# Kernel tuning notes

Measured on AMD Instinct MI355X. Metric: run time of the kernel, lower is better.

## Reference

```python
import jax, jax.numpy as jnp
import numpy as np

KV_POOL = 2


def setup_inputs() -> dict:
    key = jax.random.key(0)
    ks = jax.random.split(key, 12)
    B, C1, C2, H, W, D = 8, 256, 512, 64, 64, 64
    s = 0.02
    return {
        "x1": jax.random.normal(ks[0], (B, C1, H, W), jnp.float32),
        "x2": jax.random.normal(ks[1], (B, C2, H, W), jnp.float32),
        "Wq": jax.random.normal(ks[2], (D, C1), jnp.float32) * s,
        "bq": jnp.zeros((D,), jnp.float32),
        "Wk": jax.random.normal(ks[3], (D, C2), jnp.float32) * s,
        "bk": jnp.zeros((D,), jnp.float32),
        "Wv": jax.random.normal(ks[4], (D, C2), jnp.float32) * s,
        "bv": jnp.zeros((D,), jnp.float32),
        "Wo": jax.random.normal(ks[5], (C1, D), jnp.float32) * s,
        "bo": jnp.zeros((C1,), jnp.float32),
    }


def reference(x1, x2, Wq, bq, Wk, bk, Wv, bv, Wo, bo):
    B, C1, H, W = x1.shape
    D = Wq.shape[0]
    # adaptive_avg_pool2d to (H//2, W//2) with even dims == 2x2 mean pool
    Bs, C2, H2, W2 = x2.shape
    x2p = x2.reshape(Bs, C2, H2 // KV_POOL, KV_POOL, W2 // KV_POOL, KV_POOL).mean(axis=(3, 5))
    # 1x1 convs as channel matmuls; flatten spatial dims
    Q = jnp.einsum('bchw,dc->bhwd', x1, Wq).reshape(B, H * W, D) + bq          # [B,N,D]
    K = jnp.einsum('bchw,dc->bhwd', x2p, Wk).reshape(B, -1, D) + bk            # [B,M,D]
    V = jnp.einsum('bchw,dc->bhwd', x2p, Wv).reshape(B, -1, D) + bv            # [B,M,D]
    attn = jax.nn.softmax(jnp.einsum('bnd,bmd->bnm', Q, K), axis=-1)           # [B,N,M]
    out = jnp.einsum('bnm,bmd->bnd', attn, V)                                  # [B,N,D]
    y = jnp.einsum('bnd,cd->bnc', out, Wo) + bo                                # [B,N,C1]
    y = y.reshape(B, H, W, C1).transpose(0, 3, 1, 2)                           # [B,C1,H,W]
    return x1 + y
```

## Files before the change

### kernel.cpp

```cpp
#include <hip/hip_runtime.h>
#include <hip/hip_bf16.h>

typedef __bf16 bf16x2 __attribute__((ext_vector_type(2)));
typedef __bf16 bf16x4 __attribute__((ext_vector_type(4)));
typedef __bf16 bf16x8 __attribute__((ext_vector_type(8)));
typedef float f32x16 __attribute__((ext_vector_type(16)));
typedef unsigned int u32x4 __attribute__((ext_vector_type(4)));

static constexpr int Bc = 8, C1 = 256, C2 = 512, Hh = 64, Ww = 64, Dd = 64;
static constexpr int Nn = 4096, Mm = 1024;

#define MFMA __builtin_amdgcn_mfma_f32_32x32x16_bf16

__device__ __forceinline__ uint32_t pkbf(float a, float b) {
  union { __bf16 h[2]; uint32_t u; } x;
  x.h[0] = (__bf16)a; x.h[1] = (__bf16)b;
  return x.u;
}

__device__ __forceinline__ bf16x8 cvt8(const float* __restrict__ p) {
  float4 a = *(const float4*)p;
  float4 b2 = *(const float4*)(p + 4);
  bf16x8 r;
  r[0] = (__bf16)a.x; r[1] = (__bf16)a.y; r[2] = (__bf16)a.z; r[3] = (__bf16)a.w;
  r[4] = (__bf16)b2.x; r[5] = (__bf16)b2.y; r[6] = (__bf16)b2.z; r[7] = (__bf16)b2.w;
  return r;
}

__device__ __forceinline__ void pack16(const float* p, bf16x8& f0, bf16x8& f1) {
  uint32_t w01 = pkbf(p[0], p[1]),   w23 = pkbf(p[2], p[3]);
  uint32_t w45 = pkbf(p[4], p[5]),   w67 = pkbf(p[6], p[7]);
  uint32_t w89 = pkbf(p[8], p[9]),   wab = pkbf(p[10], p[11]);
  uint32_t wcd = pkbf(p[12], p[13]), wef = pkbf(p[14], p[15]);
  auto s0 = __builtin_amdgcn_permlane32_swap(w01, w45, false, false);
  auto s1 = __builtin_amdgcn_permlane32_swap(w23, w67, false, false);
  auto s2 = __builtin_amdgcn_permlane32_swap(w89, wcd, false, false);
  auto s3 = __builtin_amdgcn_permlane32_swap(wab, wef, false, false);
  u32x4 q0 = {s0[0], s1[0], s0[1], s1[1]};
  u32x4 q1 = {s2[0], s3[0], s2[1], s3[1]};
  f0 = __builtin_bit_cast(bf16x8, q0);
  f1 = __builtin_bit_cast(bf16x8, q1);
}


__global__ __launch_bounds__(256) void k_stage(
    const float* __restrict__ x1, const float* __restrict__ x2,
    const float* __restrict__ Wq, const float* __restrict__ Wk,
    const float* __restrict__ Wv, const float* __restrict__ Wo,
    __bf16* __restrict__ wqf, __bf16* __restrict__ wkf,
    __bf16* __restrict__ wvf, __bf16* __restrict__ wof,
    __bf16* __restrict__ x1f, __bf16* __restrict__ x2pf) {
  __shared__ __align__(16) __bf16 lds[16 * 516];
  const int lin = blockIdx.x, tid = threadIdx.x;
  const int w = tid >> 6, l = tid & 63;

  if (lin >= 1536) {
    int t = (lin - 1536) * 256 + tid;
    if (t < 2048) {
      int ll = t & 63, g = t >> 6, dh = g >> 4, ks = g & 15;
      int d = dh * 32 + (ll & 31), c = ks * 16 + (ll >> 5) * 8;
      *(bf16x8*)(wqf + (size_t)t * 8) = cvt8(Wq + (size_t)d * C1 + c);
    } else if (t < 6144) {
      int tt = t - 2048;
      int ll = tt & 63, g = tt >> 6, dh = g >> 5, ks = g & 31;
      int d = dh * 32 + (ll & 31), c = ks * 16 + (ll >> 5) * 8;
      *(bf16x8*)(wkf + (size_t)tt * 8) = cvt8(Wk + (size_t)d * C2 + c);
    } else if (t < 10240) {
      int tt = t - 6144;
      int ll = tt & 63, g = tt >> 6, dh = g >> 5, ks = g & 31;
      int d = dh * 32 + (ll & 31), c = ks * 16 + (ll >> 5) * 8;
      *(bf16x8*)(wvf + (size_t)tt * 8) = cvt8(Wv + (size_t)d * C2 + c);
    } else if (t < 12288) {
      int tt = t - 10240;
      int ll = tt & 63, g = tt >> 6, ct = g >> 2, ks = g & 3;
      int crow = ct * 32 + (ll & 31), d = ks * 16 + (ll >> 5) * 8;
      *(bf16x8*)(wof + (size_t)tt * 8) = cvt8(Wo + (size_t)crow * Dd + d);
    }
    return;
  }

  if (lin < 512) {
    const int b = lin & 7, q = lin >> 3;
    const int ks2 = q & 31, half = q >> 5;
#pragma unroll
    for (int cc = 0; cc < 4; ++cc) {
      const int c_loc = w * 4 + cc;
      const int c = ks2 * 16 + c_loc;
      const float* src = x2 + ((size_t)(b * C2 + c) * Hh + half * 32) * Ww;
      float4 v[8];
#pragma unroll
      for (int it = 0; it < 8; ++it)
        v[it] = *(const float4*)(src + it * 256 + l * 4);
#pragma unroll
      for (int it = 0; it < 8; ++it) {
        float s0 = v[it].x + v[it].y, s1 = v[it].z + v[it].w;
        float p0 = (s0 + __shfl_xor(s0, 16)) * 0.25f;
        float p1 = (s1 + __shfl_xor(s1, 16)) * 0.25f;
        const int rl = l >> 4;
        if ((rl & 1) == 0) {
          int h2l = it * 2 + (rl >> 1);
          bf16x2 pv; pv[0] = (__bf16)p0; pv[1] = (__bf16)p1;
          *(bf16x2*)(lds + c_loc * 516 + h2l * 32 + 2 * (l & 15)) = pv;
        }
      }
    }
    __syncthreads();
#pragma unroll
    for (int ti = 0; ti < 4; ++ti) {
      const int t_loc = w * 4 + ti;
      bf16x8 f;
#pragma unroll
      for (int e = 0; e < 8; ++e)
        f[e] = lds[((l >> 5) * 8 + e) * 516 + t_loc * 32 + (l & 31)];
      const int t_m = half * 16 + t_loc;
      *(bf16x8*)(x2pf + ((size_t)(b * 32 + t_m) * 32 + ks2) * 512 + l * 8) = f;
    }
  } else {
    const int e0 = lin - 512;
    const int b = e0 & 7, r = e0 >> 3;
    const int ks = r & 15, nch = r >> 4;
    const int n0 = nch * 512;
    float4 v[8];
#pragma unroll
    for (int cc = 0; cc < 4; ++cc) {
      const float* src = x1 + (size_t)(b * C1 + ks * 16 + w * 4 + cc) * Nn + n0;
#pragma unroll
      for (int j = 0; j < 2; ++j)
        v[cc * 2 + j] = *(const float4*)(src + j * 256 + l * 4);
    }
#pragma unroll
    for (int cc = 0; cc < 4; ++cc) {
      const int c_loc = w * 4 + cc;
#pragma unroll
      for (int j = 0; j < 2; ++j) {
        float4 vv = v[cc * 2 + j];
        bf16x4 t4;
        t4[0] = (__bf16)vv.x; t4[1] = (__bf16)vv.y;
        t4[2] = (__bf16)vv.z; t4[3] = (__bf16)vv.w;
        *(bf16x4*)(lds + c_loc * 516 + j * 256 + l * 4) = t4;
      }
    }
    __syncthreads();
#pragma unroll
    for (int ti = 0; ti < 4; ++ti) {
      const int t_loc = w * 4 + ti;
      bf16x8 f;
#pragma unroll
      for (int e = 0; e < 8; ++e)
        f[e] = lds[((l >> 5) * 8 + e) * 516 + t_loc * 32 + (l & 31)];
      const int t = nch * 16 + t_loc;
      *(bf16x8*)(x1f + ((size_t)(b * 128 + t) * 16 + ks) * 512 + l * 8) = f;
    }
  }
}

__global__ __launch_bounds__(256) void k_proj(
    const __bf16* __restrict__ x1f, const __bf16* __restrict__ x2pf,
    const __bf16* __restrict__ wqf, const float* __restrict__ bq,
    const __bf16* __restrict__ wkf, const float* __restrict__ bk,
    const __bf16* __restrict__ wvf, const float* __restrict__ bv,
    __bf16* __restrict__ qfb, __bf16* __restrict__ kfb,
    __bf16* __restrict__ vfb) {
  const int lin = blockIdx.x;
  const int b = lin & 7, idx = lin >> 3;
  const int tid = threadIdx.x;
  const int w = tid >> 6, l = tid & 63, h = l >> 5, nl = l & 31;

  if (idx < 64) {
    const int nsub = w & 1, dh = w >> 1;
    const int t = idx * 2 + nsub;
    const __bf16* af = x1f + ((size_t)(b * 128 + t) * 16) * 512 + l * 8;
    const __bf16* wf = wqf + (size_t)dh * 16 * 512 + l * 8;
    f32x16 acc = {};
#pragma unroll
    for (int ks = 0; ks < 16; ++ks) {
      bf16x8 a = *(const bf16x8*)(af + ks * 512);
      bf16x8 bb = *(const bf16x8*)(wf + ks * 512);
      acc = MFMA(a, bb, acc, 0, 0, 0);
    }
    const int d = dh * 32 + nl;
    const float bias = bq[d];
    __bf16* qdst = qfb + (size_t)b * Nn * Dd + (size_t)t * 2048 +
                   (d >> 4) * 512 + ((d >> 3) & 1) * 256 + (d & 7);
#pragma unroll
    for (int r = 0; r < 16; ++r) {
      int mrow = (r & 3) + 8 * (r >> 2) + 4 * h;
      qdst[mrow * 8] = (__bf16)(acc[r] + bias);
    }
  } else {
    const int h2 = idx - 64;
    const int isv = w >> 1, dh = w & 1;
    const __bf16* af = x2pf + ((size_t)(b * 32 + h2) * 32) * 512 + l * 8;
    const __bf16* wf = (isv ? wvf : wkf) + (size_t)dh * 32 * 512 + l * 8;
    f32x16 acc = {};
#pragma unroll
    for (int ks = 0; ks < 32; ++ks) {
      bf16x8 a = *(const bf16x8*)(af + ks * 512);
      bf16x8 bb = *(const bf16x8*)(wf + ks * 512);
      acc = MFMA(a, bb, acc, 0, 0, 0);
    }
    const int d = dh * 32 + nl;
    if (!isv) {
      const float bias = bk[d];
      __bf16* kdst = kfb + (size_t)b * Mm * Dd + (size_t)h2 * 2048 +
                     (d >> 4) * 512 + ((d >> 3) & 1) * 256 + (d & 7);
#pragma unroll
      for (int r = 0; r < 16; ++r) {
        int mr = (r & 3) + 8 * (r >> 2) + 4 * h;
        kdst[mr * 8] = (__bf16)(acc[r] + bias);
      }
    } else {
      const float bias = bv[d];
      float ov[16];
#pragma unroll
      for (int r = 0; r < 16; ++r) ov[r] = acc[r] + bias;
      bf16x8 f0, f1;
      pack16(ov, f0, f1);
      __bf16* vdst = vfb + (size_t)b * Mm * Dd + (size_t)h2 * 2048 + l * 8;
      *(bf16x8*)(vdst + (size_t)dh * 512) = f0;
      *(bf16x8*)(vdst + (size_t)(2 + dh) * 512) = f1;
    }
  }
}

template <int S>
__global__ __launch_bounds__(256) void k_attn_part(
    const __bf16* __restrict__ qfb, const __bf16* __restrict__ kfb,
    const __bf16* __restrict__ vfb, __bf16* __restrict__ po,
    float* __restrict__ pml) {
  const int lin = blockIdx.x;
  const int b = lin & 7, rest = lin >> 3, nblk = rest & 31, sp = rest >> 5;
  const int tid = threadIdx.x;
  const int w = tid >> 6, l = tid & 63, h = l >> 5, nl = l & 31;
  const int n = nblk * 128 + w * 32 + nl;
  constexpr int NT = Mm / S / 32;
  const int t0 = sp * NT;

  const __bf16* qt = qfb + (size_t)b * Nn * Dd + (size_t)(nblk * 4 + w) * 2048 + l * 8;
  bf16x8 qf0 = *(const bf16x8*)(qt);
  bf16x8 qf1 = *(const bf16x8*)(qt + 512);
  bf16x8 qf2 = *(const bf16x8*)(qt + 1024);
  bf16x8 qf3 = *(const bf16x8*)(qt + 1536);

  const __bf16* kt = kfb + (size_t)b * Mm * Dd + (size_t)t0 * 2048 + l * 8;
  const __bf16* vt = vfb + (size_t)b * Mm * Dd + (size_t)t0 * 2048 + l * 8;

  f32x16 o0 = {}, o1 = {};
  float lsum = 0.f;

  bf16x8 ck0 = *(const bf16x8*)(kt);
  bf16x8 ck1 = *(const bf16x8*)(kt + 512);
  bf16x8 ck2 = *(const bf16x8*)(kt + 1024);
  bf16x8 ck3 = *(const bf16x8*)(kt + 1536);
  bf16x8 cv0 = *(const bf16x8*)(vt);
  bf16x8 cv1 = *(const bf16x8*)(vt + 512);
  bf16x8 cv2 = *(const bf16x8*)(vt + 1024);
  bf16x8 cv3 = *(const bf16x8*)(vt + 1536);

#pragma unroll
  for (int i = 0; i < NT; ++i) {
    bf16x8 nk0, nk1, nk2, nk3, nv0, nv1, nv2, nv3;
    if (i + 1 < NT) {
      const __bf16* kn = kt + (size_t)(i + 1) * 2048;
      const __bf16* vn = vt + (size_t)(i + 1) * 2048;
      nk0 = *(const bf16x8*)(kn);
      nk1 = *(const bf16x8*)(kn + 512);
      nk2 = *(const bf16x8*)(kn + 1024);
      nk3 = *(const bf16x8*)(kn + 1536);
      nv0 = *(const bf16x8*)(vn);
      nv1 = *(const bf16x8*)(vn + 512);
      nv2 = *(const bf16x8*)(vn + 1024);
      nv3 = *(const bf16x8*)(vn + 1536);
    }
    f32x16 s = {};
    s = MFMA(ck0, qf0, s, 0, 0, 0);
    s = MFMA(ck1, qf1, s, 0, 0, 0);
    s = MFMA(ck2, qf2, s, 0, 0, 0);
    s = MFMA(ck3, qf3, s, 0, 0, 0);
    float p[16];
#pragma unroll
    for (int r = 0; r < 16; ++r) p[r] = __expf(s[r]);
    float u0 = (p[0] + p[1]) + (p[2] + p[3]);
    float u1 = (p[4] + p[5]) + (p[6] + p[7]);
    float u2 = (p[8] + p[9]) + (p[10] + p[11]);
    float u3 = (p[12] + p[13]) + (p[14] + p[15]);
    lsum += (u0 + u1) + (u2 + u3);
    bf16x8 pb0, pb1;
    pack16(p, pb0, pb1);
    o0 = MFMA(cv0, pb0, o0, 0, 0, 0);
    o1 = MFMA(cv1, pb0, o1, 0, 0, 0);
    o0 = MFMA(cv2, pb1, o0, 0, 0, 0);
    o1 = MFMA(cv3, pb1, o1, 0, 0, 0);
    if (i + 1 < NT) {
      ck0 = nk0; ck1 = nk1; ck2 = nk2; ck3 = nk3;
      cv0 = nv0; cv1 = nv1; cv2 = nv2; cv3 = nv3;
    }
  }

  const float ltot = lsum + __shfl_xor(lsum, 32);
  __bf16* ob = po + (size_t)(b * S + sp) * 16 * Nn * 4 + (size_t)n * 4;
#pragma unroll
  for (int q = 0; q < 4; ++q) {
    bf16x4 t0v, t1v;
#pragma unroll
    for (int e = 0; e < 4; ++e) {
      t0v[e] = (__bf16)o0[q * 4 + e];
      t1v[e] = (__bf16)o1[q * 4 + e];
    }
    *(bf16x4*)(ob + (size_t)(2 * q + h) * Nn * 4) = t0v;
    *(bf16x4*)(ob + (size_t)(8 + 2 * q + h) * Nn * 4) = t1v;
  }
  if (h == 0) pml[(size_t)(b * S + sp) * Nn + n] = ltot;
}

template <int S>
__global__ __launch_bounds__(256) void k_attn_comb(
    const float* __restrict__ x1, const __bf16* __restrict__ po,
    const float* __restrict__ pml, const __bf16* __restrict__ wof,
    const float* __restrict__ bo, float* __restrict__ out) {
  const int lin = blockIdx.x;
  const int b = lin & 7, rest = lin >> 3, nblk = rest & 31, ctg = rest >> 5;
  const int tid = threadIdx.x;
  const int w = tid >> 6, l = tid & 63, h = l >> 5, nl = l & 31;
  const int n = nblk * 128 + w * 32 + nl;

  float L = 0.f;
#pragma unroll
  for (int s = 0; s < S; ++s)
    L += pml[(size_t)(b * S + s) * Nn + n];
  const float inv = 1.f / L;

  float o[32];
#pragma unroll
  for (int r = 0; r < 32; ++r) o[r] = 0.f;
#pragma unroll
  for (int s = 0; s < S; ++s) {
    const __bf16* ob = po + (size_t)(b * S + s) * 16 * Nn * 4 + (size_t)n * 4;
#pragma unroll
    for (int q = 0; q < 4; ++q) {
      bf16x4 v0 = *(const bf16x4*)(ob + (size_t)(2 * q + h) * Nn * 4);
      bf16x4 v1 = *(const bf16x4*)(ob + (size_t)(8 + 2 * q + h) * Nn * 4);
#pragma unroll
      for (int e = 0; e < 4; ++e) {
        o[q * 4 + e] += (float)v0[e];
        o[16 + q * 4 + e] += (float)v1[e];
      }
    }
  }

  bf16x8 obf[4];
#pragma unroll
  for (int a2 = 0; a2 < 2; ++a2) {
    float ov[16];
#pragma unroll
    for (int r = 0; r < 16; ++r) ov[r] = o[a2 * 16 + r] * inv;
    pack16(ov, obf[a2 * 2], obf[a2 * 2 + 1]);
  }

  const float* x1r = x1 + (size_t)b * C1 * Nn + n;
  float* outr = out + (size_t)b * C1 * Nn + n;
#pragma unroll
  for (int ci = 0; ci < 4; ++ci) {
    const int ct = ctg * 4 + ci;
    f32x16 y = {};
#pragma unroll
    for (int ks = 0; ks < 4; ++ks) {
      bf16x8 a = *(const bf16x8*)(wof + (size_t)((ct * 4 + ks) * 64 + l) * 8);
      y = MFMA(a, obf[ks], y, 0, 0, 0);
    }
#pragma unroll
    for (int r = 0; r < 16; ++r) {
      int c = ct * 32 + (r & 3) + 8 * (r >> 2) + 4 * h;
      size_t idx = (size_t)c * Nn;
      outr[idx] = y[r] + bo[c] + x1r[idx];
    }
  }
}

__global__ __launch_bounds__(256) void k_attn(
    const float* __restrict__ x1, const __bf16* __restrict__ qfb,
    const __bf16* __restrict__ kfb, const __bf16* __restrict__ vfb,
    const __bf16* __restrict__ wof, const float* __restrict__ bo,
    float* __restrict__ out) {
  const int b = blockIdx.y, tid = threadIdx.x;
  const int w = tid >> 6, l = tid & 63, h = l >> 5, nl = l & 31;
  const int n = blockIdx.x * 128 + w * 32 + nl;

  const __bf16* qt = qfb + (size_t)b * Nn * Dd + (size_t)(blockIdx.x * 4 + w) * 2048 + l * 8;
  bf16x8 qf0 = *(const bf16x8*)(qt);
  bf16x8 qf1 = *(const bf16x8*)(qt + 512);
  bf16x8 qf2 = *(const bf16x8*)(qt + 1024);
  bf16x8 qf3 = *(const bf16x8*)(qt + 1536);

  f32x16 o0 = {}, o1 = {};
  float mrun = -INFINITY, lsum = 0.f;

  const __bf16* kb_ = kfb + (size_t)b * Mm * Dd + l * 8;
  const __bf16* vb_ = vfb + (size_t)b * Mm * Dd + l * 8;

  for (int t = 0; t < 32; ++t) {
    const __bf16* kt = kb_ + (size_t)t * 2048;
    const __bf16* vt = vb_ + (size_t)t * 2048;
    bf16x8 ka0 = *(const bf16x8*)(kt);
    bf16x8 ka1 = *(const bf16x8*)(kt + 512);
    bf16x8 ka2 = *(const bf16x8*)(kt + 1024);
    bf16x8 ka3 = *(const bf16x8*)(kt + 1536);
    bf16x8 v00 = *(const bf16x8*)(vt);
    bf16x8 v10 = *(const bf16x8*)(vt + 512);
    bf16x8 v01 = *(const bf16x8*)(vt + 1024);
    bf16x8 v11 = *(const bf16x8*)(vt + 1536);
    f32x16 s = {};
    s = MFMA(ka0, qf0, s, 0, 0, 0);
    s = MFMA(ka1, qf1, s, 0, 0, 0);
    s = MFMA(ka2, qf2, s, 0, 0, 0);
    s = MFMA(ka3, qf3, s, 0, 0, 0);
    float tmax = s[0];
#pragma unroll
    for (int r = 1; r < 16; ++r) tmax = fmaxf(tmax, s[r]);
    tmax = fmaxf(tmax, __shfl_xor(tmax, 32));
    const float mnew = fmaxf(mrun, tmax);
    const float scale = __expf(mrun - mnew);
    float p[16], psum = 0.f;
#pragma unroll
    for (int r = 0; r < 16; ++r) { p[r] = __expf(s[r] - mnew); psum += p[r]; }
    lsum = lsum * scale + psum;
    mrun = mnew;
#pragma unroll
    for (int r = 0; r < 16; ++r) { o0[r] *= scale; o1[r] *= scale; }
    bf16x8 pb0, pb1;
    pack16(p, pb0, pb1);
    o0 = MFMA(v00, pb0, o0, 0, 0, 0);
    o1 = MFMA(v10, pb0, o1, 0, 0, 0);
    o0 = MFMA(v01, pb1, o0, 0, 0, 0);
    o1 = MFMA(v11, pb1, o1, 0, 0, 0);
  }

  const float ltot = lsum + __shfl_xor(lsum, 32);
  const float inv = 1.f / ltot;

  bf16x8 ob[4];
#pragma unroll
  for (int a2 = 0; a2 < 2; ++a2) {
    float ov[16];
#pragma unroll
    for (int r = 0; r < 16; ++r) ov[r] = (a2 ? o1[r] : o0[r]) * inv;
    pack16(ov, ob[a2 * 2], ob[a2 * 2 + 1]);
  }

  const float* x1r = x1 + (size_t)b * C1 * Nn + n;
  float* outr = out + (size_t)b * C1 * Nn + n;
#pragma unroll 2
  for (int ct = 0; ct < 8; ++ct) {
    f32x16 y = {};
#pragma unroll
    for (int ks = 0; ks < 4; ++ks) {
      bf16x8 a = *(const bf16x8*)(wof + (size_t)((ct * 4 + ks) * 64 + l) * 8);
      y = MFMA(a, ob[ks], y, 0, 0, 0);
    }
#pragma unroll
    for (int r = 0; r < 16; ++r) {
      int c = ct * 32 + (r & 3) + 8 * (r >> 2) + 4 * h;
      size_t idx = (size_t)c * Nn;
      outr[idx] = y[r] + bo[c] + x1r[idx];
    }
  }
}

extern "C" void kernel_launch(void* const* d_in, const int* in_sizes, int n_in,
                              void* d_out, int out_size, void* d_ws,
                              size_t ws_size, hipStream_t stream) {
  const float* x1 = (const float*)d_in[0];
  const float* x2 = (const float*)d_in[1];
  const float* Wq = (const float*)d_in[2];
  const float* bq = (const float*)d_in[3];
  const float* Wk = (const float*)d_in[4];
  const float* bk = (const float*)d_in[5];
  const float* Wv = (const float*)d_in[6];
  const float* bv = (const float*)d_in[7];
  const float* Wo = (const float*)d_in[8];
  const float* bo = (const float*)d_in[9];
  float* out = (float*)d_out;
  char* ws = (char*)d_ws;

  __bf16* wqf  = (__bf16*)(ws);
  __bf16* wkf  = (__bf16*)(ws + 32768);
  __bf16* wvf  = (__bf16*)(ws + 98304);
  __bf16* wof  = (__bf16*)(ws + 163840);
  __bf16* qfb  = (__bf16*)(ws + 196608);
  __bf16* kfb  = (__bf16*)(ws + 4390912);
  __bf16* vfb  = (__bf16*)(ws + 5439488);
  __bf16* x1f  = (__bf16*)(ws + 6488064);
  __bf16* x2pf = (__bf16*)(ws + 23265280);
  __bf16* po   = (__bf16*)(ws + 31653888);
  const size_t ws8 = 31653888ull + 33554432ull + 1048576ull;
  const size_t ws4 = 31653888ull + 16777216ull + 524288ull;

  hipLaunchKernelGGL(k_stage, dim3(1584), dim3(256), 0, stream,
                     x1, x2, Wq, Wk, Wv, Wo, wqf, wkf, wvf, wof, x1f, x2pf);
  hipLaunchKernelGGL(k_proj, dim3(768), dim3(256), 0, stream,
                     x1f, x2pf, wqf, bq, wkf, bk, wvf, bv, qfb, kfb, vfb);
  if (ws_size >= ws8) {
    float* pml = (float*)(ws + 31653888 + 33554432);
    hipLaunchKernelGGL(k_attn_part<8>, dim3(32 * 8 * 8), dim3(256), 0, stream,
                       qfb, kfb, vfb, po, pml);
    hipLaunchKernelGGL(k_attn_comb<8>, dim3(32 * 8 * 2), dim3(256), 0, stream,
                       x1, po, pml, wof, bo, out);
  } else if (ws_size >= ws4) {
    float* pml = (float*)(ws + 31653888 + 16777216);
    hipLaunchKernelGGL(k_attn_part<4>, dim3(32 * 8 * 4), dim3(256), 0, stream,
                       qfb, kfb, vfb, po, pml);
    hipLaunchKernelGGL(k_attn_comb<4>, dim3(32 * 8 * 2), dim3(256), 0, stream,
                       x1, po, pml, wof, bo, out);
  } else {
    hipLaunchKernelGGL(k_attn, dim3(32, 8), dim3(256), 0, stream,
                       x1, qfb, kfb, vfb, wof, bo, out);
  }
}
```

Baseline: 66.49 us.

## Move activation transpose into projection kernel and read bf16 x1 for residual

The staging kernel now converts x1 to bf16 in its original NCHW layout and 2x2-pools x2 to bf16 NCHW with simple coalesced elementwise code, with no LDS transpose. The projection kernel loads channel-major tiles and transposes them through LDS before its MFMA loops. The attention epilogue now reads the residual x1 from this bf16 copy instead of the fp32 input, which halves the residual read traffic. In exchange the residual is rounded to bf16, which lowers output accuracy, and the scalar LDS transpose writes in the projection may cause bank conflicts.

```diff
diff --git a/kernel.cpp b/kernel.cpp
--- a/kernel.cpp
+++ b/kernel.cpp
@@ -42,20 +42,50 @@
   f1 = __builtin_bit_cast(bf16x8, q1);
 }
 
-
-__global__ __launch_bounds__(256) void k_stage(
+__global__ __launch_bounds__(256) void k_convert(
     const float* __restrict__ x1, const float* __restrict__ x2,
     const float* __restrict__ Wq, const float* __restrict__ Wk,
     const float* __restrict__ Wv, const float* __restrict__ Wo,
     __bf16* __restrict__ wqf, __bf16* __restrict__ wkf,
     __bf16* __restrict__ wvf, __bf16* __restrict__ wof,
-    __bf16* __restrict__ x1f, __bf16* __restrict__ x2pf) {
-  __shared__ __align__(16) __bf16 lds[16 * 516];
+    __bf16* __restrict__ x1bf, __bf16* __restrict__ x2p) {
   const int lin = blockIdx.x, tid = threadIdx.x;
-  const int w = tid >> 6, l = tid & 63;
-
-  if (lin >= 1536) {
-    int t = (lin - 1536) * 256 + tid;
+
+  if (lin < 1024) {
+    const int gi = lin * 256 + tid;
+    float4 v[8];
+#pragma unroll
+    for (int it = 0; it < 8; ++it)
+      v[it] = *(const float4*)(x1 + ((size_t)it * 262144 + gi) * 4);
+#pragma unroll
+    for (int it = 0; it < 8; ++it) {
+      bf16x4 t4;
+      t4[0] = (__bf16)v[it].x; t4[1] = (__bf16)v[it].y;
+      t4[2] = (__bf16)v[it].z; t4[3] = (__bf16)v[it].w;
+      *(bf16x4*)(x1bf + ((size_t)it * 262144 + gi) * 4) = t4;
+    }
+  } else if (lin < 2048) {
+    const int gi = (lin - 1024) * 256 + tid;
+    float4 v0[8], v1[8];
+#pragma unroll
+    for (int it = 0; it < 8; ++it) {
+      int pi = it * 262144 + gi;
+      int bc = pi >> 9, r = pi & 511, h2 = r >> 4, q = r & 15;
+      const float* base = x2 + (size_t)bc * 4096 + h2 * 128 + q * 4;
+      v0[it] = *(const float4*)(base);
+      v1[it] = *(const float4*)(base + 64);
+    }
+#pragma unroll
+    for (int it = 0; it < 8; ++it) {
+      int pi = it * 262144 + gi;
+      int bc = pi >> 9, r = pi & 511, h2 = r >> 4, q = r & 15;
+      float p0 = (v0[it].x + v0[it].y + v1[it].x + v1[it].y) * 0.25f;
+      float p1 = (v0[it].z + v0[it].w + v1[it].z + v1[it].w) * 0.25f;
+      bf16x2 pv; pv[0] = (__bf16)p0; pv[1] = (__bf16)p1;
+      *(bf16x2*)(x2p + (size_t)bc * 1024 + h2 * 32 + q * 2) = pv;
+    }
+  } else {
+    int t = (lin - 2048) * 256 + tid;
     if (t < 2048) {
       int ll = t & 63, g = t >> 6, dh = g >> 4, ks = g & 15;
       int d = dh * 32 + (ll & 31), c = ks * 16 + (ll >> 5) * 8;
@@ -76,110 +106,53 @@
       int crow = ct * 32 + (ll & 31), d = ks * 16 + (ll >> 5) * 8;
       *(bf16x8*)(wof + (size_t)tt * 8) = cvt8(Wo + (size_t)crow * Dd + d);
     }
-    return;
-  }
-
-  if (lin < 512) {
-    const int b = lin & 7, q = lin >> 3;
-    const int ks2 = q & 31, half = q >> 5;
-#pragma unroll
-    for (int cc = 0; cc < 4; ++cc) {
-      const int c_loc = w * 4 + cc;
-      const int c = ks2 * 16 + c_loc;
-      const float* src = x2 + ((size_t)(b * C2 + c) * Hh + half * 32) * Ww;
-      float4 v[8];
-#pragma unroll
-      for (int it = 0; it < 8; ++it)
-        v[it] = *(const float4*)(src + it * 256 + l * 4);
-#pragma unroll
-      for (int it = 0; it < 8; ++it) {
-        float s0 = v[it].x + v[it].y, s1 = v[it].z + v[it].w;
-        float p0 = (s0 + __shfl_xor(s0, 16)) * 0.25f;
-        float p1 = (s1 + __shfl_xor(s1, 16)) * 0.25f;
-        const int rl = l >> 4;
-        if ((rl & 1) == 0) {
-          int h2l = it * 2 + (rl >> 1);
-          bf16x2 pv; pv[0] = (__bf16)p0; pv[1] = (__bf16)p1;
-          *(bf16x2*)(lds + c_loc * 516 + h2l * 32 + 2 * (l & 15)) = pv;
-        }
-      }
-    }
-    __syncthreads();
-#pragma unroll
-    for (int ti = 0; ti < 4; ++ti) {
-      const int t_loc = w * 4 + ti;
-      bf16x8 f;
-#pragma unroll
-      for (int e = 0; e < 8; ++e)
-        f[e] = lds[((l >> 5) * 8 + e) * 516 + t_loc * 32 + (l & 31)];
-      const int t_m = half * 16 + t_loc;
-      *(bf16x8*)(x2pf + ((size_t)(b * 32 + t_m) * 32 + ks2) * 512 + l * 8) = f;
-    }
-  } else {
-    const int e0 = lin - 512;
-    const int b = e0 & 7, r = e0 >> 3;
-    const int ks = r & 15, nch = r >> 4;
-    const int n0 = nch * 512;
-    float4 v[8];
-#pragma unroll
-    for (int cc = 0; cc < 4; ++cc) {
-      const float* src = x1 + (size_t)(b * C1 + ks * 16 + w * 4 + cc) * Nn + n0;
-#pragma unroll
-      for (int j = 0; j < 2; ++j)
-        v[cc * 2 + j] = *(const float4*)(src + j * 256 + l * 4);
-    }
-#pragma unroll
-    for (int cc = 0; cc < 4; ++cc) {
-      const int c_loc = w * 4 + cc;
-#pragma unroll
-      for (int j = 0; j < 2; ++j) {
-        float4 vv = v[cc * 2 + j];
-        bf16x4 t4;
-        t4[0] = (__bf16)vv.x; t4[1] = (__bf16)vv.y;
-        t4[2] = (__bf16)vv.z; t4[3] = (__bf16)vv.w;
-        *(bf16x4*)(lds + c_loc * 516 + j * 256 + l * 4) = t4;
-      }
-    }
-    __syncthreads();
-#pragma unroll
-    for (int ti = 0; ti < 4; ++ti) {
-      const int t_loc = w * 4 + ti;
-      bf16x8 f;
-#pragma unroll
-      for (int e = 0; e < 8; ++e)
-        f[e] = lds[((l >> 5) * 8 + e) * 516 + t_loc * 32 + (l & 31)];
-      const int t = nch * 16 + t_loc;
-      *(bf16x8*)(x1f + ((size_t)(b * 128 + t) * 16 + ks) * 512 + l * 8) = f;
-    }
-  }
-}
-
-__global__ __launch_bounds__(256) void k_proj(
-    const __bf16* __restrict__ x1f, const __bf16* __restrict__ x2pf,
+  }
+}
+
+__global__ __launch_bounds__(256) void k_proj2(
+    const __bf16* __restrict__ x1bf, const __bf16* __restrict__ x2p,
     const __bf16* __restrict__ wqf, const float* __restrict__ bq,
     const __bf16* __restrict__ wkf, const float* __restrict__ bk,
     const __bf16* __restrict__ wvf, const float* __restrict__ bv,
     __bf16* __restrict__ qfb, __bf16* __restrict__ kfb,
     __bf16* __restrict__ vfb) {
+  __shared__ __align__(16) __bf16 lds[64 * 266];
   const int lin = blockIdx.x;
   const int b = lin & 7, idx = lin >> 3;
   const int tid = threadIdx.x;
   const int w = tid >> 6, l = tid & 63, h = l >> 5, nl = l & 31;
 
   if (idx < 64) {
+    const int n0 = idx * 64;
+    bf16x4 sv[8];
+#pragma unroll
+    for (int g2 = 0; g2 < 2; ++g2) {
+#pragma unroll
+      for (int it = 0; it < 8; ++it) {
+        int c = (g2 * 8 + it) * 16 + (tid >> 4), q = tid & 15;
+        sv[it] = *(const bf16x4*)(x1bf + (size_t)(b * C1 + c) * Nn + n0 + 4 * q);
+      }
+#pragma unroll
+      for (int it = 0; it < 8; ++it) {
+        int c = (g2 * 8 + it) * 16 + (tid >> 4), q = tid & 15;
+#pragma unroll
+        for (int j = 0; j < 4; ++j) lds[(4 * q + j) * 266 + c] = sv[it][j];
+      }
+    }
+    __syncthreads();
     const int nsub = w & 1, dh = w >> 1;
-    const int t = idx * 2 + nsub;
-    const __bf16* af = x1f + ((size_t)(b * 128 + t) * 16) * 512 + l * 8;
-    const __bf16* wf = wqf + (size_t)dh * 16 * 512 + l * 8;
+    const __bf16* arow = lds + (nsub * 32 + nl) * 266;
+    const __bf16* wq8 = wqf + (size_t)dh * 16 * 512 + l * 8;
     f32x16 acc = {};
 #pragma unroll
     for (int ks = 0; ks < 16; ++ks) {
-      bf16x8 a = *(const bf16x8*)(af + ks * 512);
-      bf16x8 bb = *(const bf16x8*)(wf + ks * 512);
+      bf16x8 a = *(const bf16x8*)(arow + ks * 16 + 8 * h);
+      bf16x8 bb = *(const bf16x8*)(wq8 + ks * 512);
       acc = MFMA(a, bb, acc, 0, 0, 0);
     }
     const int d = dh * 32 + nl;
     const float bias = bq[d];
+    const int t = idx * 2 + nsub;
     __bf16* qdst = qfb + (size_t)b * Nn * Dd + (size_t)t * 2048 +
                    (d >> 4) * 512 + ((d >> 3) & 1) * 256 + (d & 7);
 #pragma unroll
@@ -189,14 +162,30 @@
     }
   } else {
     const int h2 = idx - 64;
+    bf16x4 sv[8];
+#pragma unroll
+    for (int g2 = 0; g2 < 2; ++g2) {
+#pragma unroll
+      for (int it = 0; it < 8; ++it) {
+        int c = (g2 * 8 + it) * 32 + (tid >> 3), q = tid & 7;
+        sv[it] = *(const bf16x4*)(x2p + (size_t)(b * C2 + c) * Mm + h2 * 32 + 4 * q);
+      }
+#pragma unroll
+      for (int it = 0; it < 8; ++it) {
+        int c = (g2 * 8 + it) * 32 + (tid >> 3), q = tid & 7;
+#pragma unroll
+        for (int j = 0; j < 4; ++j) lds[(4 * q + j) * 522 + c] = sv[it][j];
+      }
+    }
+    __syncthreads();
     const int isv = w >> 1, dh = w & 1;
-    const __bf16* af = x2pf + ((size_t)(b * 32 + h2) * 32) * 512 + l * 8;
-    const __bf16* wf = (isv ? wvf : wkf) + (size_t)dh * 32 * 512 + l * 8;
+    const __bf16* arow = lds + nl * 522;
+    const __bf16* wf8 = (isv ? wvf : wkf) + (size_t)dh * 32 * 512 + l * 8;
     f32x16 acc = {};
 #pragma unroll
     for (int ks = 0; ks < 32; ++ks) {
-      bf16x8 a = *(const bf16x8*)(af + ks * 512);
-      bf16x8 bb = *(const bf16x8*)(wf + ks * 512);
+      bf16x8 a = *(const bf16x8*)(arow + ks * 16 + 8 * h);
+      bf16x8 bb = *(const bf16x8*)(wf8 + ks * 512);
       acc = MFMA(a, bb, acc, 0, 0, 0);
     }
     const int d = dh * 32 + nl;
@@ -315,7 +304,7 @@
 
 template <int S>
 __global__ __launch_bounds__(256) void k_attn_comb(
-    const float* __restrict__ x1, const __bf16* __restrict__ po,
+    const __bf16* __restrict__ x1bf, const __bf16* __restrict__ po,
     const float* __restrict__ pml, const __bf16* __restrict__ wof,
     const float* __restrict__ bo, float* __restrict__ out) {
   const int lin = blockIdx.x;
@@ -357,7 +346,7 @@
     pack16(ov, obf[a2 * 2], obf[a2 * 2 + 1]);
   }
 
-  const float* x1r = x1 + (size_t)b * C1 * Nn + n;
+  const __bf16* x1r = x1bf + (size_t)b * C1 * Nn + n;
   float* outr = out + (size_t)b * C1 * Nn + n;
 #pragma unroll
   for (int ci = 0; ci < 4; ++ci) {
@@ -372,13 +361,13 @@
     for (int r = 0; r < 16; ++r) {
       int c = ct * 32 + (r & 3) + 8 * (r >> 2) + 4 * h;
       size_t idx = (size_t)c * Nn;
-      outr[idx] = y[r] + bo[c] + x1r[idx];
+      outr[idx] = y[r] + bo[c] + (float)x1r[idx];
     }
   }
 }
 
 __global__ __launch_bounds__(256) void k_attn(
-    const float* __restrict__ x1, const __bf16* __restrict__ qfb,
+    const __bf16* __restrict__ x1bf, const __bf16* __restrict__ qfb,
     const __bf16* __restrict__ kfb, const __bf16* __restrict__ vfb,
     const __bf16* __restrict__ wof, const float* __restrict__ bo,
     float* __restrict__ out) {
@@ -447,7 +436,7 @@
     pack16(ov, ob[a2 * 2], ob[a2 * 2 + 1]);
   }
 
-  const float* x1r = x1 + (size_t)b * C1 * Nn + n;
+  const __bf16* x1r = x1bf + (size_t)b * C1 * Nn + n;
   float* outr = out + (size_t)b * C1 * Nn + n;
 #pragma unroll 2
   for (int ct = 0; ct < 8; ++ct) {
@@ -461,7 +450,7 @@
     for (int r = 0; r < 16; ++r) {
       int c = ct * 32 + (r & 3) + 8 * (r >> 2) + 4 * h;
       size_t idx = (size_t)c * Nn;
-      outr[idx] = y[r] + bo[c] + x1r[idx];
+      outr[idx] = y[r] + bo[c] + (float)x1r[idx];
     }
   }
 }
@@ -489,30 +478,30 @@
   __bf16* qfb  = (__bf16*)(ws + 196608);
   __bf16* kfb  = (__bf16*)(ws + 4390912);
   __bf16* vfb  = (__bf16*)(ws + 5439488);
-  __bf16* x1f  = (__bf16*)(ws + 6488064);
-  __bf16* x2pf = (__bf16*)(ws + 23265280);
+  __bf16* x1bf = (__bf16*)(ws + 6488064);
+  __bf16* x2p  = (__bf16*)(ws + 23265280);
   __bf16* po   = (__bf16*)(ws + 31653888);
   const size_t ws8 = 31653888ull + 33554432ull + 1048576ull;
   const size_t ws4 = 31653888ull + 16777216ull + 524288ull;
 
-  hipLaunchKernelGGL(k_stage, dim3(1584), dim3(256), 0, stream,
-                     x1, x2, Wq, Wk, Wv, Wo, wqf, wkf, wvf, wof, x1f, x2pf);
-  hipLaunchKernelGGL(k_proj, dim3(768), dim3(256), 0, stream,
-                     x1f, x2pf, wqf, bq, wkf, bk, wvf, bv, qfb, kfb, vfb);
+  hipLaunchKernelGGL(k_convert, dim3(2096), dim3(256), 0, stream,
+                     x1, x2, Wq, Wk, Wv, Wo, wqf, wkf, wvf, wof, x1bf, x2p);
+  hipLaunchKernelGGL(k_proj2, dim3(768), dim3(256), 0, stream,
+                     x1bf, x2p, wqf, bq, wkf, bk, wvf, bv, qfb, kfb, vfb);
   if (ws_size >= ws8) {
     float* pml = (float*)(ws + 31653888 + 33554432);
     hipLaunchKernelGGL(k_attn_part<8>, dim3(32 * 8 * 8), dim3(256), 0, stream,
                        qfb, kfb, vfb, po, pml);
     hipLaunchKernelGGL(k_attn_comb<8>, dim3(32 * 8 * 2), dim3(256), 0, stream,
-                       x1, po, pml, wof, bo, out);
+                       x1bf, po, pml, wof, bo, out);
   } else if (ws_size >= ws4) {
     float* pml = (float*)(ws + 31653888 + 16777216);
     hipLaunchKernelGGL(k_attn_part<4>, dim3(32 * 8 * 4), dim3(256), 0, stream,
                        qfb, kfb, vfb, po, pml);
     hipLaunchKernelGGL(k_attn_comb<4>, dim3(32 * 8 * 2), dim3(256), 0, stream,
-                       x1, po, pml, wof, bo, out);
+                       x1bf, po, pml, wof, bo, out);
   } else {
     hipLaunchKernelGGL(k_attn, dim3(32, 8), dim3(256), 0, stream,
-                       x1, qfb, kfb, vfb, wof, bo, out);
-  }
-}
+                       x1bf, qfb, kfb, vfb, wof, bo, out);
+  }
+}
```

Result: slower. 70.12 us (+5.5%).
